# Optimization experiments

Hardware: AMD Instinct MI355X
Metric: run time of the kernel (lower is better)

The kernel has to match this reference:

```python
import jax, jax.numpy as jnp
import numpy as np

T, B, I, H, O = 512, 64, 512, 1024, 512
STDV = 1.0 / np.sqrt(H)


def setup_inputs() -> dict:
    key = jax.random.key(0)
    ks = jax.random.split(key, 12)
    u = lambda k, shape: jax.random.uniform(k, shape, jnp.float32, -STDV, STDV)
    return {
        "input": jax.random.normal(ks[0], (T, B, I), jnp.float32),
        "state": jnp.zeros((B, H), jnp.float32),
        "W_zh": u(ks[1], (H, H)), "W_zx": u(ks[2], (I, H)), "b_z": u(ks[3], (H,)),
        "W_rh": u(ks[4], (H, H)), "W_rx": u(ks[5], (I, H)), "b_r": u(ks[6], (H,)),
        "W_hh": u(ks[7], (H, H)), "W_hx": u(ks[8], (I, H)), "b_h": u(ks[9], (H,)),
        "W_out": u(ks[10], (O, H)), "b_out": u(ks[11], (O,)),
    }


def reference(input, state, W_zh, W_zx, b_z, W_rh, W_rx, b_r, W_hh, W_hx, b_h, W_out, b_out):
    # input: [T, B, I]; state: [B, H]
    def step(h, x):
        z = jax.nn.sigmoid(h @ W_zh + x @ W_zx + b_z)
        r = jax.nn.sigmoid(h @ W_rh + x @ W_rx + b_r)
        ht = jnp.tanh((h * r) @ W_hh + x @ W_hx + b_h)
        h = (1.0 - z) * h + z * ht
        y = h @ W_out.T + b_out  # Linear(hidim -> outdim)
        return h, y

    h_final, Y = jax.lax.scan(step, state, input)  # Y: [T, B, O]
    # torch.cat(Y, dim=0) -> [T*B, O]
    return Y.reshape(T * B, O), h_final
```

## Files before the change

kernel.cpp:

```cpp
#include <hip/hip_runtime.h>
#include <cstdint>


#define TT 512
#define BB 64
#define II 512
#define HH 1024
#define OO 512
#define NTHR 512

typedef float4 f4;
__device__ __forceinline__ f4 ld4(const float* p){ return *reinterpret_cast<const f4*>(p); }
__device__ __forceinline__ int swz(int k){ return k ^ (((k >> 4) & 7) << 2); }

__device__ __forceinline__ void ldc16(const float* p, f4* d){
  asm volatile(
    "global_load_dwordx4 %0,  %16, off sc0 sc1\n\t"
    "global_load_dwordx4 %1,  %16, off offset:256 sc0 sc1\n\t"
    "global_load_dwordx4 %2,  %16, off offset:512 sc0 sc1\n\t"
    "global_load_dwordx4 %3,  %16, off offset:768 sc0 sc1\n\t"
    "global_load_dwordx4 %4,  %16, off offset:1024 sc0 sc1\n\t"
    "global_load_dwordx4 %5,  %16, off offset:1280 sc0 sc1\n\t"
    "global_load_dwordx4 %6,  %16, off offset:1536 sc0 sc1\n\t"
    "global_load_dwordx4 %7,  %16, off offset:1792 sc0 sc1\n\t"
    "global_load_dwordx4 %8,  %16, off offset:2048 sc0 sc1\n\t"
    "global_load_dwordx4 %9,  %16, off offset:2304 sc0 sc1\n\t"
    "global_load_dwordx4 %10, %16, off offset:2560 sc0 sc1\n\t"
    "global_load_dwordx4 %11, %16, off offset:2816 sc0 sc1\n\t"
    "global_load_dwordx4 %12, %16, off offset:3072 sc0 sc1\n\t"
    "global_load_dwordx4 %13, %16, off offset:3328 sc0 sc1\n\t"
    "global_load_dwordx4 %14, %16, off offset:3584 sc0 sc1\n\t"
    "s_waitcnt vmcnt(1)\n\t"
    "global_load_dwordx4 %15, %16, off offset:3840 sc0 sc1\n\t"
    "s_waitcnt vmcnt(0)"
    : "=&v"(d[0]),"=&v"(d[1]),"=&v"(d[2]),"=&v"(d[3]),
      "=&v"(d[4]),"=&v"(d[5]),"=&v"(d[6]),"=&v"(d[7]),
      "=&v"(d[8]),"=&v"(d[9]),"=&v"(d[10]),"=&v"(d[11]),
      "=&v"(d[12]),"=&v"(d[13]),"=&v"(d[14]),"=&v"(d[15])
    : "v"(p) : "memory");
}
__device__ __forceinline__ void stc1(float* p, float v){
  asm volatile("global_store_dword %0, %1, off sc0 sc1" :: "v"(p), "v"(v) : "memory");
}

__global__ void k_transpose_x(const float* __restrict__ x, float* __restrict__ xT){
  size_t total = (size_t)TT * II * BB;
  for (size_t n = (size_t)blockIdx.x * blockDim.x + threadIdx.x; n < total;
       n += (size_t)gridDim.x * blockDim.x){
    size_t t = n / ((size_t)II * BB);
    size_t rem = n % ((size_t)II * BB);
    size_t i = rem / BB, b = rem % BB;
    xT[n] = x[(t * BB + b) * II + i];
  }
}

__global__ void k_transpose_wx(const float* __restrict__ W, float* __restrict__ WT){
  size_t n = (size_t)blockIdx.x * blockDim.x + threadIdx.x;
  if (n >= (size_t)II * HH) return;
  size_t j = n / II, k = n % II;
  WT[n] = W[k * HH + j];
}

__global__ void k_transpose_h0(const float* __restrict__ st, float* __restrict__ h0){
  size_t n = (size_t)blockIdx.x * blockDim.x + threadIdx.x;
  if (n >= (size_t)HH * BB) return;
  size_t j = n / BB, b = n % BB;
  h0[n] = st[b * HH + j];
}

__global__ void k_init_bars(unsigned* bars){
  if (threadIdx.x < 512) bars[threadIdx.x] = 0;
}

__device__ __forceinline__ void g_arrive(unsigned* bars, int g, int jt, unsigned ep){
  asm volatile("s_waitcnt vmcnt(0)" ::: "memory");
  unsigned* leaf = bars + (g * 9 + (jt & 7)) * 16;
  unsigned old = __hip_atomic_fetch_add(leaf, 1u, __ATOMIC_RELAXED, __HIP_MEMORY_SCOPE_AGENT);
  if (old + 1u == ep * 16u)
    __hip_atomic_fetch_add(bars + (g * 9 + 8) * 16, 1u, __ATOMIC_RELAXED, __HIP_MEMORY_SCOPE_AGENT);
}
__device__ __forceinline__ void g_wait(unsigned* bars, int g, unsigned ep){
  unsigned* root = bars + (g * 9 + 8) * 16;
  while (__hip_atomic_load(root, __ATOMIC_RELAXED, __HIP_MEMORY_SCOPE_AGENT) < ep * 8u)
    __builtin_amdgcn_s_sleep(1);
}

#define WREDUCE(v) { v += __shfl_xor(v, 8); v += __shfl_xor(v, 16); v += __shfl_xor(v, 32); }

__global__ __launch_bounds__(NTHR, 2) void k_gru(
    const float* __restrict__ xT,
    const float* __restrict__ WxTr, const float* __restrict__ WxTz, const float* __restrict__ WxTh,
    float* __restrict__ h, float* __restrict__ s,
    const float* __restrict__ W_zh, const float* __restrict__ b_z,
    const float* __restrict__ W_rh, const float* __restrict__ b_r,
    const float* __restrict__ W_hh, const float* __restrict__ b_h,
    const float* __restrict__ W_out, const float* __restrict__ b_out,
    float* __restrict__ out, unsigned* __restrict__ bars)
{
  __shared__ float sW[3 * 8 * 1024];
  __shared__ float red[8 * 528];
  __shared__ float xpre[3][256];
  __shared__ float sZ[256];
  __shared__ float hloc[16][32];
  __shared__ float sBias[32];

  const int tid = threadIdx.x;
  const int bid = blockIdx.x;
  const int jt = bid & 127, bhalf = bid >> 7;
  const int j0 = jt * 8, o0 = jt * 4, bbase = bhalf * 32;
  const int jrow = (jt & 1) * 8;

  #pragma unroll
  for (int kk2 = 0; kk2 < 2; ++kk2){
    const int k = tid * 2 + kk2;
    f4 vr  = ld4(W_rh + (size_t)k * HH + j0);
    f4 vr2 = ld4(W_rh + (size_t)k * HH + j0 + 4);
    f4 vz  = ld4(W_zh + (size_t)k * HH + j0);
    f4 vz2 = ld4(W_zh + (size_t)k * HH + j0 + 4);
    f4 vh  = ld4(W_hh + (size_t)k * HH + j0);
    f4 vh2 = ld4(W_hh + (size_t)k * HH + j0 + 4);
    const int kx = swz(k);
    float ar[8] = {vr.x,vr.y,vr.z,vr.w,vr2.x,vr2.y,vr2.z,vr2.w};
    float az[8] = {vz.x,vz.y,vz.z,vz.w,vz2.x,vz2.y,vz2.z,vz2.w};
    float ah[8] = {vh.x,vh.y,vh.z,vh.w,vh2.x,vh2.y,vh2.z,vh2.w};
    #pragma unroll
    for (int c = 0; c < 8; ++c){
      sW[0*8192 + c*1024 + kx] = ar[c];
      sW[1*8192 + c*1024 + kx] = az[c];
      sW[2*8192 + c*1024 + kx] = ah[c];
    }
  }
  if (tid < 8){
    sBias[tid]      = b_r[j0 + tid];
    sBias[8 + tid]  = b_z[j0 + tid];
    sBias[16 + tid] = b_h[j0 + tid];
    if (tid < 4) sBias[24 + tid] = b_out[o0 + tid];
  }

  const int bg = tid & 7, b0 = bbase + bg * 4;
  const int ksec = tid >> 3;
  const int wv = tid >> 6;
  const bool wr0 = ((tid & 56) == 0);
  const int kh0 = ksec * 16;
  const int kx0 = ksec * 8;
  const bool own = (ksec == (jt >> 1));
  __syncthreads();

  for (int t = -1; t < TT; ++t){
    f4 st4[16];
    if (t >= 0){
      float aR[8][4] = {};
      ldc16(h + kh0 * BB + b0, st4);
      if (own){
        #pragma unroll
        for (int kk = 0; kk < 16; ++kk)
          *reinterpret_cast<f4*>(&hloc[kk][bg*4]) = st4[kk];
      }
      #pragma unroll
      for (int i4 = 0; i4 < 4; ++i4){
        const int kxc = swz(kh0 + i4*4);
        #pragma unroll
        for (int c = 0; c < 8; ++c){
          f4 wf = *reinterpret_cast<const f4*>(&sW[0*8192 + c*1024 + kxc]);
          float wvv[4] = {wf.x, wf.y, wf.z, wf.w};
          #pragma unroll
          for (int kk = 0; kk < 4; ++kk){
            const f4 hv = st4[i4*4+kk];
            aR[c][0] = fmaf(wvv[kk], hv.x, aR[c][0]);
            aR[c][1] = fmaf(wvv[kk], hv.y, aR[c][1]);
            aR[c][2] = fmaf(wvv[kk], hv.z, aR[c][2]);
            aR[c][3] = fmaf(wvv[kk], hv.w, aR[c][3]);
          }
        }
      }
      #pragma unroll
      for (int c = 0; c < 8; ++c)
        #pragma unroll
        for (int bb = 0; bb < 4; ++bb) WREDUCE(aR[c][bb]);
      if (wr0)
        #pragma unroll
        for (int c = 0; c < 8; ++c)
          #pragma unroll
          for (int bb = 0; bb < 4; ++bb)
            red[wv*528 + c*32 + bg*4 + bb] = aR[c][bb];
      __syncthreads();
      if (tid < 256){
        float sum = 0.f;
        #pragma unroll
        for (int w = 0; w < 8; ++w) sum += red[w*528 + tid];
        const int c = tid >> 5, bl = tid & 31;
        const float v = sum + xpre[0][tid] + sBias[c];
        const float rr = 1.f / (1.f + expf(-v));
        stc1(&s[(j0 + c)*BB + bbase + bl], rr * hloc[jrow + c][bl]);
      }
      __syncthreads();
      if (tid == 0) g_arrive(bars, bhalf, jt, 2*t + 1);

      float aZ[8][4] = {};
      float aY[4][4] = {};
      #pragma unroll
      for (int i4 = 0; i4 < 4; ++i4){
        const int kc = kh0 + i4*4;
        const int kxc = swz(kc);
        #pragma unroll
        for (int c = 0; c < 8; ++c){
          f4 wf = *reinterpret_cast<const f4*>(&sW[1*8192 + c*1024 + kxc]);
          float wvv[4] = {wf.x, wf.y, wf.z, wf.w};
          #pragma unroll
          for (int kk = 0; kk < 4; ++kk){
            const f4 hv = st4[i4*4+kk];
            aZ[c][0] = fmaf(wvv[kk], hv.x, aZ[c][0]);
            aZ[c][1] = fmaf(wvv[kk], hv.y, aZ[c][1]);
            aZ[c][2] = fmaf(wvv[kk], hv.z, aZ[c][2]);
            aZ[c][3] = fmaf(wvv[kk], hv.w, aZ[c][3]);
          }
        }
        #pragma unroll
        for (int oc = 0; oc < 4; ++oc){
          f4 wo = ld4(W_out + (size_t)(o0 + oc) * HH + kc);
          float wvv[4] = {wo.x, wo.y, wo.z, wo.w};
          #pragma unroll
          for (int kk = 0; kk < 4; ++kk){
            const f4 hv = st4[i4*4+kk];
            aY[oc][0] = fmaf(wvv[kk], hv.x, aY[oc][0]);
            aY[oc][1] = fmaf(wvv[kk], hv.y, aY[oc][1]);
            aY[oc][2] = fmaf(wvv[kk], hv.z, aY[oc][2]);
            aY[oc][3] = fmaf(wvv[kk], hv.w, aY[oc][3]);
          }
        }
      }
      #pragma unroll
      for (int c = 0; c < 8; ++c)
        #pragma unroll
        for (int bb = 0; bb < 4; ++bb) WREDUCE(aZ[c][bb]);
      #pragma unroll
      for (int oc = 0; oc < 4; ++oc)
        #pragma unroll
        for (int bb = 0; bb < 4; ++bb) WREDUCE(aY[oc][bb]);
      if (wr0){
        #pragma unroll
        for (int c = 0; c < 8; ++c)
          #pragma unroll
          for (int bb = 0; bb < 4; ++bb)
            red[wv*528 + c*32 + bg*4 + bb] = aZ[c][bb];
        #pragma unroll
        for (int oc = 0; oc < 4; ++oc)
          #pragma unroll
          for (int bb = 0; bb < 4; ++bb)
            red[wv*528 + 256 + oc*32 + bg*4 + bb] = aY[oc][bb];
      }
      __syncthreads();
      if (tid < 256){
        float sum = 0.f;
        #pragma unroll
        for (int w = 0; w < 8; ++w) sum += red[w*528 + tid];
        const int c = tid >> 5;
        sZ[tid] = 1.f / (1.f + expf(-(sum + xpre[1][tid] + sBias[8 + c])));
      } else if (tid < 384){
        const int idx = tid - 256;
        float sum = 0.f;
        #pragma unroll
        for (int w = 0; w < 8; ++w) sum += red[w*528 + tid];
        const int oc = idx >> 5, bl = idx & 31;
        if (t > 0)
          out[((size_t)(t-1)*BB + bbase + bl)*OO + o0 + oc] = sum + sBias[24 + oc];
      }
      if (tid == 0) g_wait(bars, bhalf, 2*t + 1);
      __syncthreads();

      float aH[8][4] = {};
      f4 sv16[16];
      ldc16(s + kh0 * BB + b0, sv16);
      #pragma unroll
      for (int i4 = 0; i4 < 4; ++i4){
        const int kxc = swz(kh0 + i4*4);
        #pragma unroll
        for (int c = 0; c < 8; ++c){
          f4 wf = *reinterpret_cast<const f4*>(&sW[2*8192 + c*1024 + kxc]);
          float wvv[4] = {wf.x, wf.y, wf.z, wf.w};
          #pragma unroll
          for (int kk = 0; kk < 4; ++kk){
            const f4 sv = sv16[i4*4+kk];
            aH[c][0] = fmaf(wvv[kk], sv.x, aH[c][0]);
            aH[c][1] = fmaf(wvv[kk], sv.y, aH[c][1]);
            aH[c][2] = fmaf(wvv[kk], sv.z, aH[c][2]);
            aH[c][3] = fmaf(wvv[kk], sv.w, aH[c][3]);
          }
        }
      }
      #pragma unroll
      for (int c = 0; c < 8; ++c)
        #pragma unroll
        for (int bb = 0; bb < 4; ++bb) WREDUCE(aH[c][bb]);
      if (wr0)
        #pragma unroll
        for (int c = 0; c < 8; ++c)
          #pragma unroll
          for (int bb = 0; bb < 4; ++bb)
            red[wv*528 + c*32 + bg*4 + bb] = aH[c][bb];
      __syncthreads();
      if (tid < 256){
        float sum = 0.f;
        #pragma unroll
        for (int w = 0; w < 8; ++w) sum += red[w*528 + tid];
        const int c = tid >> 5, bl = tid & 31;
        const float ht = tanhf(sum + xpre[2][tid] + sBias[16 + c]);
        const float z = sZ[tid];
        const float hold = hloc[jrow + c][bl];
        const float hnew = fmaf(z, ht - hold, hold);
        stc1(&h[(j0 + c)*BB + bbase + bl], hnew);
        if (t == TT - 1) out[(size_t)TT*BB*OO + (size_t)(bbase + bl)*HH + j0 + c] = hnew;
      }
      __syncthreads();
      if (tid == 0) g_arrive(bars, bhalf, jt, 2*t + 2);
    }

    if (t + 1 < TT){
      const int tc = t + 1;
      float aXr[8][4] = {}, aXz[8][4] = {}, aXh[8][4] = {};
      const float* xb = xT + (size_t)tc * II * BB + kx0 * BB + b0;
      #pragma unroll
      for (int i4 = 0; i4 < 2; ++i4){
        f4 xv4[4];
        #pragma unroll
        for (int kk = 0; kk < 4; ++kk) xv4[kk] = ld4(xb + (i4*4+kk) * BB);
        #pragma unroll
        for (int c = 0; c < 8; ++c){
          f4 wr_ = ld4(WxTr + (size_t)(j0 + c) * II + kx0 + i4*4);
          f4 wz_ = ld4(WxTz + (size_t)(j0 + c) * II + kx0 + i4*4);
          f4 wh_ = ld4(WxTh + (size_t)(j0 + c) * II + kx0 + i4*4);
          float wrv[4] = {wr_.x, wr_.y, wr_.z, wr_.w};
          float wzv[4] = {wz_.x, wz_.y, wz_.z, wz_.w};
          float whv[4] = {wh_.x, wh_.y, wh_.z, wh_.w};
          #pragma unroll
          for (int kk = 0; kk < 4; ++kk){
            const f4 xv = xv4[kk];
            aXr[c][0] = fmaf(wrv[kk], xv.x, aXr[c][0]);
            aXr[c][1] = fmaf(wrv[kk], xv.y, aXr[c][1]);
            aXr[c][2] = fmaf(wrv[kk], xv.z, aXr[c][2]);
            aXr[c][3] = fmaf(wrv[kk], xv.w, aXr[c][3]);
            aXz[c][0] = fmaf(wzv[kk], xv.x, aXz[c][0]);
            aXz[c][1] = fmaf(wzv[kk], xv.y, aXz[c][1]);
            aXz[c][2] = fmaf(wzv[kk], xv.z, aXz[c][2]);
            aXz[c][3] = fmaf(wzv[kk], xv.w, aXz[c][3]);
            aXh[c][0] = fmaf(whv[kk], xv.x, aXh[c][0]);
            aXh[c][1] = fmaf(whv[kk], xv.y, aXh[c][1]);
            aXh[c][2] = fmaf(whv[kk], xv.z, aXh[c][2]);
            aXh[c][3] = fmaf(whv[kk], xv.w, aXh[c][3]);
          }
        }
      }
      #pragma unroll
      for (int c = 0; c < 8; ++c)
        #pragma unroll
        for (int bb = 0; bb < 4; ++bb){ WREDUCE(aXr[c][bb]); WREDUCE(aXz[c][bb]); WREDUCE(aXh[c][bb]); }
      if (wr0)
        #pragma unroll
        for (int c = 0; c < 8; ++c)
          #pragma unroll
          for (int bb = 0; bb < 4; ++bb){
            red[wv*528 + c*32 + bg*4 + bb]       = aXr[c][bb];
            red[wv*528 + 256 + c*32 + bg*4 + bb] = aXz[c][bb];
          }
      __syncthreads();
      {
        float sum = 0.f;
        #pragma unroll
        for (int w = 0; w < 8; ++w) sum += red[w*528 + tid];
        if (tid < 256) xpre[0][tid] = sum;
        else           xpre[1][tid - 256] = sum;
      }
      __syncthreads();
      if (wr0)
        #pragma unroll
        for (int c = 0; c < 8; ++c)
          #pragma unroll
          for (int bb = 0; bb < 4; ++bb)
            red[wv*528 + c*32 + bg*4 + bb] = aXh[c][bb];
      __syncthreads();
      if (tid < 256){
        float sum = 0.f;
        #pragma unroll
        for (int w = 0; w < 8; ++w) sum += red[w*528 + tid];
        xpre[2][tid] = sum;
      }
      __syncthreads();
    }

    if (t >= 0){
      if (tid == 0) g_wait(bars, bhalf, 2*t + 2);
      __syncthreads();
    }
  }

  {
    float aY[4][4] = {};
    f4 hv16[16];
    ldc16(h + kh0 * BB + b0, hv16);
    #pragma unroll
    for (int i4 = 0; i4 < 4; ++i4){
      const int kc = kh0 + i4*4;
      #pragma unroll
      for (int oc = 0; oc < 4; ++oc){
        f4 wo = ld4(W_out + (size_t)(o0 + oc) * HH + kc);
        float wvv[4] = {wo.x, wo.y, wo.z, wo.w};
        #pragma unroll
        for (int kk = 0; kk < 4; ++kk){
          const f4 hv = hv16[i4*4+kk];
          aY[oc][0] = fmaf(wvv[kk], hv.x, aY[oc][0]);
          aY[oc][1] = fmaf(wvv[kk], hv.y, aY[oc][1]);
          aY[oc][2] = fmaf(wvv[kk], hv.z, aY[oc][2]);
          aY[oc][3] = fmaf(wvv[kk], hv.w, aY[oc][3]);
        }
      }
    }
    #pragma unroll
    for (int oc = 0; oc < 4; ++oc)
      #pragma unroll
      for (int bb = 0; bb < 4; ++bb) WREDUCE(aY[oc][bb]);
    if (wr0)
      #pragma unroll
      for (int oc = 0; oc < 4; ++oc)
        #pragma unroll
        for (int bb = 0; bb < 4; ++bb)
          red[wv*528 + oc*32 + bg*4 + bb] = aY[oc][bb];
    __syncthreads();
    if (tid < 128){
      float sum = 0.f;
      #pragma unroll
      for (int w = 0; w < 8; ++w) sum += red[w*528 + tid];
      const int oc = tid >> 5, bl = tid & 31;
      out[((size_t)(TT-1)*BB + bbase + bl)*OO + o0 + oc] = sum + sBias[24 + oc];
    }
  }
}

extern "C" void kernel_launch(void* const* d_in, const int* in_sizes, int n_in,
                              void* d_out, int out_size, void* d_ws, size_t ws_size,
                              hipStream_t stream) {
  const float* x     = (const float*)d_in[0];
  const float* st    = (const float*)d_in[1];
  const float* W_zh  = (const float*)d_in[2];
  const float* W_zx  = (const float*)d_in[3];
  const float* b_z   = (const float*)d_in[4];
  const float* W_rh  = (const float*)d_in[5];
  const float* W_rx  = (const float*)d_in[6];
  const float* b_r   = (const float*)d_in[7];
  const float* W_hh  = (const float*)d_in[8];
  const float* W_hx  = (const float*)d_in[9];
  const float* b_h   = (const float*)d_in[10];
  const float* W_out = (const float*)d_in[11];
  const float* b_out = (const float*)d_in[12];
  float* out = (float*)d_out;
  float* ws  = (float*)d_ws;

  const size_t xT_sz = (size_t)TT * II * BB;
  const size_t wx_sz = (size_t)II * HH;
  const size_t h_sz  = (size_t)HH * BB;
  const size_t need  = (xT_sz + 3*wx_sz + 2*h_sz) * sizeof(float) + 512*sizeof(unsigned);
  if (ws_size < need) return;

  float* xT   = ws;
  float* WxTr = xT + xT_sz;
  float* WxTz = WxTr + wx_sz;
  float* WxTh = WxTz + wx_sz;
  float* h    = WxTh + wx_sz;
  float* s    = h + h_sz;
  unsigned* bars = (unsigned*)(s + h_sz);

  k_transpose_x <<<8192, 256, 0, stream>>>(x, xT);
  k_transpose_wx<<<2048, 256, 0, stream>>>(W_rx, WxTr);
  k_transpose_wx<<<2048, 256, 0, stream>>>(W_zx, WxTz);
  k_transpose_wx<<<2048, 256, 0, stream>>>(W_hx, WxTh);
  k_transpose_h0<<< 256, 256, 0, stream>>>(st, h);
  k_init_bars   <<<   1, 512, 0, stream>>>(bars);

  k_gru<<<256, NTHR, 0, stream>>>(xT, WxTr, WxTz, WxTh, h, s,
                                  W_zh, b_z, W_rh, b_r, W_hh, b_h,
                                  W_out, b_out, out, bars);
}
```

Measured before the change: 12.98 ms.

## Split input projections per gate and overlap them with grid-barrier waits

The fused three-gate input-projection block for step t+1 is split into three per-gate pieces. Each piece is scheduled into a latency gap: the z-gate one after issuing the s load, the h-gate one between arrive and wait on the second grid barrier, and the r-gate one after issuing the next h load. The coherent state loads are split into issue and wait so that global load latency and barrier spin time overlap with independent input-projection work. In exchange there are more block-level syncs and reduction passes per step, and the new xpre writes must be checked for races against the readers of the same buffers.

```diff
diff --git a/kernel.cpp b/kernel.cpp
--- a/kernel.cpp
+++ b/kernel.cpp
@@ -13,7 +13,7 @@
 __device__ __forceinline__ f4 ld4(const float* p){ return *reinterpret_cast<const f4*>(p); }
 __device__ __forceinline__ int swz(int k){ return k ^ (((k >> 4) & 7) << 2); }
 
-__device__ __forceinline__ void ldc16(const float* p, f4* d){
+__device__ __forceinline__ void ldc16_issue(const float* p, f4* d){
   asm volatile(
     "global_load_dwordx4 %0,  %16, off sc0 sc1\n\t"
     "global_load_dwordx4 %1,  %16, off offset:256 sc0 sc1\n\t"
@@ -30,14 +30,18 @@
     "global_load_dwordx4 %12, %16, off offset:3072 sc0 sc1\n\t"
     "global_load_dwordx4 %13, %16, off offset:3328 sc0 sc1\n\t"
     "global_load_dwordx4 %14, %16, off offset:3584 sc0 sc1\n\t"
-    "s_waitcnt vmcnt(1)\n\t"
-    "global_load_dwordx4 %15, %16, off offset:3840 sc0 sc1\n\t"
-    "s_waitcnt vmcnt(0)"
+    "global_load_dwordx4 %15, %16, off offset:3840 sc0 sc1"
     : "=&v"(d[0]),"=&v"(d[1]),"=&v"(d[2]),"=&v"(d[3]),
       "=&v"(d[4]),"=&v"(d[5]),"=&v"(d[6]),"=&v"(d[7]),
       "=&v"(d[8]),"=&v"(d[9]),"=&v"(d[10]),"=&v"(d[11]),
       "=&v"(d[12]),"=&v"(d[13]),"=&v"(d[14]),"=&v"(d[15])
     : "v"(p) : "memory");
+}
+#define WAITALL() do { asm volatile("s_waitcnt vmcnt(0)" ::: "memory"); \
+                       __builtin_amdgcn_sched_barrier(0); } while (0)
+__device__ __forceinline__ void ldc16(const float* p, f4* d){
+  ldc16_issue(p, d);
+  asm volatile("s_waitcnt vmcnt(0)" ::: "memory");
 }
 __device__ __forceinline__ void stc1(float* p, float v){
   asm volatile("global_store_dword %0, %1, off sc0 sc1" :: "v"(p), "v"(v) : "memory");
@@ -146,16 +150,66 @@
   const bool own = (ksec == (jt >> 1));
   __syncthreads();
 
-  for (int t = -1; t < TT; ++t){
-    f4 st4[16];
-    if (t >= 0){
+  #define XPRE_G(g_, tc_) do {                                               \
+    float aX_[8][4] = {};                                                    \
+    const float* xb_ = xT + (size_t)(tc_) * II * BB + kx0 * BB + b0;         \
+    const float* Wg_ = ((g_) == 0) ? WxTr : ((g_) == 1) ? WxTz : WxTh;       \
+    _Pragma("unroll")                                                        \
+    for (int i4 = 0; i4 < 2; ++i4){                                          \
+      f4 xv4_[4];                                                            \
+      _Pragma("unroll")                                                      \
+      for (int kk = 0; kk < 4; ++kk) xv4_[kk] = ld4(xb_ + (i4*4+kk) * BB);   \
+      _Pragma("unroll")                                                      \
+      for (int c = 0; c < 8; ++c){                                           \
+        f4 wf_ = ld4(Wg_ + (size_t)(j0 + c) * II + kx0 + i4*4);              \
+        float wvv_[4] = {wf_.x, wf_.y, wf_.z, wf_.w};                        \
+        _Pragma("unroll")                                                    \
+        for (int kk = 0; kk < 4; ++kk){                                      \
+          const f4 xv_ = xv4_[kk];                                           \
+          aX_[c][0] = fmaf(wvv_[kk], xv_.x, aX_[c][0]);                      \
+          aX_[c][1] = fmaf(wvv_[kk], xv_.y, aX_[c][1]);                      \
+          aX_[c][2] = fmaf(wvv_[kk], xv_.z, aX_[c][2]);                      \
+          aX_[c][3] = fmaf(wvv_[kk], xv_.w, aX_[c][3]);                      \
+        }                                                                    \
+      }                                                                      \
+    }                                                                        \
+    _Pragma("unroll")                                                        \
+    for (int c = 0; c < 8; ++c)                                              \
+      _Pragma("unroll")                                                      \
+      for (int bb = 0; bb < 4; ++bb) WREDUCE(aX_[c][bb]);                    \
+    if (wr0)                                                                 \
+      _Pragma("unroll")                                                      \
+      for (int c = 0; c < 8; ++c)                                            \
+        _Pragma("unroll")                                                    \
+        for (int bb = 0; bb < 4; ++bb)                                       \
+          red[wv*528 + c*32 + bg*4 + bb] = aX_[c][bb];                       \
+    __syncthreads();                                                         \
+    if (tid < 256){                                                          \
+      float sum_ = 0.f;                                                      \
+      _Pragma("unroll")                                                      \
+      for (int w = 0; w < 8; ++w) sum_ += red[w*528 + tid];                  \
+      xpre[g_][tid] = sum_;                                                  \
+    }                                                                        \
+    __syncthreads();                                                         \
+  } while (0)
+
+  f4 st4[16];
+  f4 sv16[16];
+
+  XPRE_G(1, 0);
+  XPRE_G(2, 0);
+  XPRE_G(0, 0);
+  ldc16_issue(h + kh0 * BB + b0, st4);
+
+  for (int t = 0; t < TT; ++t){
+    WAITALL();
+    if (own){
+      #pragma unroll
+      for (int kk = 0; kk < 16; ++kk)
+        *reinterpret_cast<f4*>(&hloc[kk][bg*4]) = st4[kk];
+    }
+    {
       float aR[8][4] = {};
-      ldc16(h + kh0 * BB + b0, st4);
-      if (own){
-        #pragma unroll
-        for (int kk = 0; kk < 16; ++kk)
-          *reinterpret_cast<f4*>(&hloc[kk][bg*4]) = st4[kk];
-      }
       #pragma unroll
       for (int i4 = 0; i4 < 4; ++i4){
         const int kxc = swz(kh0 + i4*4);
@@ -183,19 +237,21 @@
           #pragma unroll
           for (int bb = 0; bb < 4; ++bb)
             red[wv*528 + c*32 + bg*4 + bb] = aR[c][bb];
-      __syncthreads();
-      if (tid < 256){
-        float sum = 0.f;
-        #pragma unroll
-        for (int w = 0; w < 8; ++w) sum += red[w*528 + tid];
-        const int c = tid >> 5, bl = tid & 31;
-        const float v = sum + xpre[0][tid] + sBias[c];
-        const float rr = 1.f / (1.f + expf(-v));
-        stc1(&s[(j0 + c)*BB + bbase + bl], rr * hloc[jrow + c][bl]);
-      }
-      __syncthreads();
-      if (tid == 0) g_arrive(bars, bhalf, jt, 2*t + 1);
-
+    }
+    __syncthreads();
+    if (tid < 256){
+      float sum = 0.f;
+      #pragma unroll
+      for (int w = 0; w < 8; ++w) sum += red[w*528 + tid];
+      const int c = tid >> 5, bl = tid & 31;
+      const float v = sum + xpre[0][tid] + sBias[c];
+      const float rr = 1.f / (1.f + expf(-v));
+      stc1(&s[(j0 + c)*BB + bbase + bl], rr * hloc[jrow + c][bl]);
+    }
+    __syncthreads();
+    if (tid == 0) g_arrive(bars, bhalf, jt, 2*t + 1);
+
+    {
       float aZ[8][4] = {};
       float aY[4][4] = {};
       #pragma unroll
@@ -249,28 +305,32 @@
           for (int bb = 0; bb < 4; ++bb)
             red[wv*528 + 256 + oc*32 + bg*4 + bb] = aY[oc][bb];
       }
-      __syncthreads();
-      if (tid < 256){
-        float sum = 0.f;
-        #pragma unroll
-        for (int w = 0; w < 8; ++w) sum += red[w*528 + tid];
-        const int c = tid >> 5;
-        sZ[tid] = 1.f / (1.f + expf(-(sum + xpre[1][tid] + sBias[8 + c])));
-      } else if (tid < 384){
-        const int idx = tid - 256;
-        float sum = 0.f;
-        #pragma unroll
-        for (int w = 0; w < 8; ++w) sum += red[w*528 + tid];
-        const int oc = idx >> 5, bl = idx & 31;
-        if (t > 0)
-          out[((size_t)(t-1)*BB + bbase + bl)*OO + o0 + oc] = sum + sBias[24 + oc];
-      }
-      if (tid == 0) g_wait(bars, bhalf, 2*t + 1);
-      __syncthreads();
-
+    }
+    __syncthreads();
+    if (tid < 256){
+      float sum = 0.f;
+      #pragma unroll
+      for (int w = 0; w < 8; ++w) sum += red[w*528 + tid];
+      const int c = tid >> 5;
+      sZ[tid] = 1.f / (1.f + expf(-(sum + xpre[1][tid] + sBias[8 + c])));
+    } else if (tid < 384){
+      const int idx = tid - 256;
+      float sum = 0.f;
+      #pragma unroll
+      for (int w = 0; w < 8; ++w) sum += red[w*528 + tid];
+      const int oc = idx >> 5, bl = idx & 31;
+      if (t > 0)
+        out[((size_t)(t-1)*BB + bbase + bl)*OO + o0 + oc] = sum + sBias[24 + oc];
+    }
+    if (tid == 0) g_wait(bars, bhalf, 2*t + 1);
+    __syncthreads();
+
+    ldc16_issue(s + kh0 * BB + b0, sv16);
+    if (t + 1 < TT) XPRE_G(1, t + 1);
+    WAITALL();
+
+    {
       float aH[8][4] = {};
-      f4 sv16[16];
-      ldc16(s + kh0 * BB + b0, sv16);
       #pragma unroll
       for (int i4 = 0; i4 < 4; ++i4){
         const int kxc = swz(kh0 + i4*4);
@@ -298,98 +358,30 @@
           #pragma unroll
           for (int bb = 0; bb < 4; ++bb)
             red[wv*528 + c*32 + bg*4 + bb] = aH[c][bb];
-      __syncthreads();
-      if (tid < 256){
-        float sum = 0.f;
-        #pragma unroll
-        for (int w = 0; w < 8; ++w) sum += red[w*528 + tid];
-        const int c = tid >> 5, bl = tid & 31;
-        const float ht = tanhf(sum + xpre[2][tid] + sBias[16 + c]);
-        const float z = sZ[tid];
-        const float hold = hloc[jrow + c][bl];
-        const float hnew = fmaf(z, ht - hold, hold);
-        stc1(&h[(j0 + c)*BB + bbase + bl], hnew);
-        if (t == TT - 1) out[(size_t)TT*BB*OO + (size_t)(bbase + bl)*HH + j0 + c] = hnew;
-      }
-      __syncthreads();
-      if (tid == 0) g_arrive(bars, bhalf, jt, 2*t + 2);
-    }
+    }
+    __syncthreads();
+    if (tid < 256){
+      float sum = 0.f;
+      #pragma unroll
+      for (int w = 0; w < 8; ++w) sum += red[w*528 + tid];
+      const int c = tid >> 5, bl = tid & 31;
+      const float ht = tanhf(sum + xpre[2][tid] + sBias[16 + c]);
+      const float z = sZ[tid];
+      const float hold = hloc[jrow + c][bl];
+      const float hnew = fmaf(z, ht - hold, hold);
+      stc1(&h[(j0 + c)*BB + bbase + bl], hnew);
+      if (t == TT - 1) out[(size_t)TT*BB*OO + (size_t)(bbase + bl)*HH + j0 + c] = hnew;
+    }
+    __syncthreads();
+    if (tid == 0) g_arrive(bars, bhalf, jt, 2*t + 2);
+
+    if (t + 1 < TT) XPRE_G(2, t + 1);
+    if (tid == 0) g_wait(bars, bhalf, 2*t + 2);
+    __syncthreads();
 
     if (t + 1 < TT){
-      const int tc = t + 1;
-      float aXr[8][4] = {}, aXz[8][4] = {}, aXh[8][4] = {};
-      const float* xb = xT + (size_t)tc * II * BB + kx0 * BB + b0;
-      #pragma unroll
-      for (int i4 = 0; i4 < 2; ++i4){
-        f4 xv4[4];
-        #pragma unroll
-        for (int kk = 0; kk < 4; ++kk) xv4[kk] = ld4(xb + (i4*4+kk) * BB);
-        #pragma unroll
-        for (int c = 0; c < 8; ++c){
-          f4 wr_ = ld4(WxTr + (size_t)(j0 + c) * II + kx0 + i4*4);
-          f4 wz_ = ld4(WxTz + (size_t)(j0 + c) * II + kx0 + i4*4);
-          f4 wh_ = ld4(WxTh + (size_t)(j0 + c) * II + kx0 + i4*4);
-          float wrv[4] = {wr_.x, wr_.y, wr_.z, wr_.w};
-          float wzv[4] = {wz_.x, wz_.y, wz_.z, wz_.w};
-          float whv[4] = {wh_.x, wh_.y, wh_.z, wh_.w};
-          #pragma unroll
-          for (int kk = 0; kk < 4; ++kk){
-            const f4 xv = xv4[kk];
-            aXr[c][0] = fmaf(wrv[kk], xv.x, aXr[c][0]);
-            aXr[c][1] = fmaf(wrv[kk], xv.y, aXr[c][1]);
-            aXr[c][2] = fmaf(wrv[kk], xv.z, aXr[c][2]);
-            aXr[c][3] = fmaf(wrv[kk], xv.w, aXr[c][3]);
-            aXz[c][0] = fmaf(wzv[kk], xv.x, aXz[c][0]);
-            aXz[c][1] = fmaf(wzv[kk], xv.y, aXz[c][1]);
-            aXz[c][2] = fmaf(wzv[kk], xv.z, aXz[c][2]);
-            aXz[c][3] = fmaf(wzv[kk], xv.w, aXz[c][3]);
-            aXh[c][0] = fmaf(whv[kk], xv.x, aXh[c][0]);
-            aXh[c][1] = fmaf(whv[kk], xv.y, aXh[c][1]);
-            aXh[c][2] = fmaf(whv[kk], xv.z, aXh[c][2]);
-            aXh[c][3] = fmaf(whv[kk], xv.w, aXh[c][3]);
-          }
-        }
-      }
-      #pragma unroll
-      for (int c = 0; c < 8; ++c)
-        #pragma unroll
-        for (int bb = 0; bb < 4; ++bb){ WREDUCE(aXr[c][bb]); WREDUCE(aXz[c][bb]); WREDUCE(aXh[c][bb]); }
-      if (wr0)
-        #pragma unroll
-        for (int c = 0; c < 8; ++c)
-          #pragma unroll
-          for (int bb = 0; bb < 4; ++bb){
-            red[wv*528 + c*32 + bg*4 + bb]       = aXr[c][bb];
-            red[wv*528 + 256 + c*32 + bg*4 + bb] = aXz[c][bb];
-          }
-      __syncthreads();
-      {
-        float sum = 0.f;
-        #pragma unroll
-        for (int w = 0; w < 8; ++w) sum += red[w*528 + tid];
-        if (tid < 256) xpre[0][tid] = sum;
-        else           xpre[1][tid - 256] = sum;
-      }
-      __syncthreads();
-      if (wr0)
-        #pragma unroll
-        for (int c = 0; c < 8; ++c)
-          #pragma unroll
-          for (int bb = 0; bb < 4; ++bb)
-            red[wv*528 + c*32 + bg*4 + bb] = aXh[c][bb];
-      __syncthreads();
-      if (tid < 256){
-        float sum = 0.f;
-        #pragma unroll
-        for (int w = 0; w < 8; ++w) sum += red[w*528 + tid];
-        xpre[2][tid] = sum;
-      }
-      __syncthreads();
-    }
-
-    if (t >= 0){
-      if (tid == 0) g_wait(bars, bhalf, 2*t + 2);
-      __syncthreads();
+      ldc16_issue(h + kh0 * BB + b0, st4);
+      XPRE_G(0, t + 1);
     }
   }
 
@@ -433,6 +425,7 @@
       out[((size_t)(TT-1)*BB + bbase + bl)*OO + o0 + oc] = sum + sBias[24 + oc];
     }
   }
+  #undef XPRE_G
 }
 
 extern "C" void kernel_launch(void* const* d_in, const int* in_sizes, int n_in,
```

New measurement: 16.05 ms. 1.24x slower.
